# Kernel optimization log

Measured on AMD Instinct MI355X. Metric: run time of the kernel, lower is better.

## Reference

```python
import jax, jax.numpy as jnp
import numpy as np

WIN_SIZE = 256
PATCH_SIZE = [8]
CHANNEL = 32
B_CH = 256        # B_outer(8) * CHANNEL(32)
H, E = 8, 64


def _attn(q, k):
    # q, k: [B*ch, L, H, E] -> softmax scores [B*ch, H, L, L]
    scale = 1.0 / jnp.sqrt(jnp.asarray(E, q.dtype))
    scores = jnp.einsum('blhe,bshe->bhls', q, k) * scale
    return jax.nn.softmax(scores, axis=-1)  # dropout is identity in eval


def _channel_mean(a):
    # '(b reduce_b) l m n -> b l m n' mean with reduce_b=CHANNEL (channel innermost)
    bc, h, m, n = a.shape
    return a.reshape(bc // CHANNEL, CHANNEL, h, m, n).mean(axis=1)


def setup_inputs() -> dict:
    key = jax.random.key(0)
    k1, k2, k3, k4 = jax.random.split(key, 4)
    p = PATCH_SIZE[0]
    patch_num = WIN_SIZE // p
    return {
        'queries_patch_size': jax.random.normal(k1, (B_CH, patch_num, H, E), jnp.float32),
        'keys_patch_size':    jax.random.normal(k2, (B_CH, patch_num, H, E), jnp.float32),
        'queries_patch_num':  jax.random.normal(k3, (B_CH, p, H, E), jnp.float32),
        'keys_patch_num':     jax.random.normal(k4, (B_CH, p, H, E), jnp.float32),
        'patch_index': 0,
        'attn_mask': 0,
    }


def reference(queries_patch_size, keys_patch_size, queries_patch_num, keys_patch_num, patch_index, attn_mask):
    p = PATCH_SIZE[patch_index]
    rep = WIN_SIZE // p

    # patch_size branch: element-wise repeat (einops repeat) then channel mean.
    # mean over channel commutes with the repeat, so reduce first (same math,
    # avoids the 536MB intermediate the torch code materializes).
    s_ps = _channel_mean(_attn(queries_patch_size, keys_patch_size))  # [B,H,rep,rep]
    s_ps = jnp.repeat(jnp.repeat(s_ps, p, axis=2), p, axis=3)

    # patch_num branch: torch .repeat == tile, then channel mean (also commutes).
    s_pn = _channel_mean(_attn(queries_patch_num, keys_patch_num))    # [B,H,p,p]
    s_pn = jnp.tile(s_pn, (1, 1, rep, rep))

    return (s_ps, s_pn)
```

## Files before the change

kernel.cpp:

```cpp
#include <hip/hip_runtime.h>
#include <stdint.h>


__global__ __launch_bounds__(256)
void scores_kernel(const float* __restrict__ qps,
                   const float* __restrict__ kps,
                   const float* __restrict__ qpn,
                   const float* __restrict__ kpn,
                   float* __restrict__ ws_ps,
                   float* __restrict__ ws_pn)
{
    __shared__ float red[4][32 * 36];
    const int tid  = threadIdx.x;
    const int wv   = tid >> 6;
    const int lane = tid & 63;
    const int blk  = blockIdx.x;

    if (blk < 512) {
        const int a     = blk >> 3;
        const int chunk = blk & 7;
        const int bo = a >> 3, h = a & 7;
        const int ch = chunk * 4 + wv;
        const int b  = bo * 32 + ch;
        const int i = lane >> 3, j = lane & 7;

        const float4* Q = reinterpret_cast<const float4*>(qps) + ((b * 32 + 4 * i) * 8 + h) * 16;
        const float4* K = reinterpret_cast<const float4*>(kps) + ((b * 32 + 4 * j) * 8 + h) * 16;

        float acc[4][4];
        #pragma unroll
        for (int r = 0; r < 4; ++r)
            #pragma unroll
            for (int c = 0; c < 4; ++c) acc[r][c] = 0.f;

        #pragma unroll 4
        for (int c = 0; c < 16; ++c) {
            float4 q[4], k[4];
            #pragma unroll
            for (int r = 0; r < 4; ++r) { q[r] = Q[r * 128 + c]; k[r] = K[r * 128 + c]; }
            #pragma unroll
            for (int r = 0; r < 4; ++r)
                #pragma unroll
                for (int u = 0; u < 4; ++u) {
                    acc[r][u] = fmaf(q[r].x, k[u].x, acc[r][u]);
                    acc[r][u] = fmaf(q[r].y, k[u].y, acc[r][u]);
                    acc[r][u] = fmaf(q[r].z, k[u].z, acc[r][u]);
                    acc[r][u] = fmaf(q[r].w, k[u].w, acc[r][u]);
                }
        }

        #pragma unroll
        for (int r = 0; r < 4; ++r) {
            float v0 = acc[r][0] * 0.125f, v1 = acc[r][1] * 0.125f;
            float v2 = acc[r][2] * 0.125f, v3 = acc[r][3] * 0.125f;
            float m = fmaxf(fmaxf(v0, v1), fmaxf(v2, v3));
            m = fmaxf(m, __shfl_xor(m, 1));
            m = fmaxf(m, __shfl_xor(m, 2));
            m = fmaxf(m, __shfl_xor(m, 4));
            float e0 = __expf(v0 - m), e1 = __expf(v1 - m);
            float e2 = __expf(v2 - m), e3 = __expf(v3 - m);
            float s = (e0 + e1) + (e2 + e3);
            s += __shfl_xor(s, 1);
            s += __shfl_xor(s, 2);
            s += __shfl_xor(s, 4);
            const float inv = 1.f / (s * 32.f);
            float4 p; p.x = e0 * inv; p.y = e1 * inv; p.z = e2 * inv; p.w = e3 * inv;
            *reinterpret_cast<float4*>(&red[wv][(4 * i + r) * 36 + 4 * j]) = p;
        }
        __syncthreads();

        const int l = tid >> 3, s4 = (tid & 7) * 4;
        const float4 u0 = *reinterpret_cast<const float4*>(&red[0][l * 36 + s4]);
        const float4 u1 = *reinterpret_cast<const float4*>(&red[1][l * 36 + s4]);
        const float4 u2 = *reinterpret_cast<const float4*>(&red[2][l * 36 + s4]);
        const float4 u3 = *reinterpret_cast<const float4*>(&red[3][l * 36 + s4]);
        float* dst = ws_ps + a * 1024 + tid * 4;
        unsafeAtomicAdd(dst + 0, (u0.x + u1.x) + (u2.x + u3.x));
        unsafeAtomicAdd(dst + 1, (u0.y + u1.y) + (u2.y + u3.y));
        unsafeAtomicAdd(dst + 2, (u0.z + u1.z) + (u2.z + u3.z));
        unsafeAtomicAdd(dst + 3, (u0.w + u1.w) + (u2.w + u3.w));
    } else {
        const int pid = (blk - 512) * 4 + wv;
        const int b = pid >> 3, h = pid & 7;
        const int i = lane >> 3, j = lane & 7;
        const float4* qv = reinterpret_cast<const float4*>(qpn) + ((b * 8 + i) * 8 + h) * 16;
        const float4* kv = reinterpret_cast<const float4*>(kpn) + ((b * 8 + j) * 8 + h) * 16;

        float acc = 0.f;
        #pragma unroll
        for (int c = 0; c < 16; ++c) {
            float4 q = qv[c], k = kv[c];
            acc = fmaf(q.x, k.x, acc);
            acc = fmaf(q.y, k.y, acc);
            acc = fmaf(q.z, k.z, acc);
            acc = fmaf(q.w, k.w, acc);
        }
        const float s = acc * 0.125f;
        float m = s;
        m = fmaxf(m, __shfl_xor(m, 1));
        m = fmaxf(m, __shfl_xor(m, 2));
        m = fmaxf(m, __shfl_xor(m, 4));
        float e = __expf(s - m);
        float sum = e;
        sum += __shfl_xor(sum, 1);
        sum += __shfl_xor(sum, 2);
        sum += __shfl_xor(sum, 4);
        unsafeAtomicAdd(ws_pn + ((b >> 5) * 8 + h) * 64 + lane, e / (sum * 32.f));
    }
}

__global__ __launch_bounds__(256)
void writer_kernel(const float* __restrict__ ws_ps,
                   const float* __restrict__ ws_pn,
                   float* __restrict__ out)
{
    const int g = blockIdx.x * 256 + threadIdx.x;
    float4* o4 = reinterpret_cast<float4*>(out);
    if (g < 1048576) {
        const int a  = g >> 14;
        const int r  = g & 16383;
        const int i  = r >> 6;
        const int j4 = r & 63;
        const float v = ws_ps[a * 1024 + (i >> 3) * 32 + (j4 >> 1)];
        float4 o; o.x = v; o.y = v; o.z = v; o.w = v;
        o4[g] = o;
    } else {
        const int g2 = g - 1048576;
        const int a  = g2 >> 14;
        const int r  = g2 & 16383;
        const int i  = r >> 6;
        const int j4 = r & 63;
        o4[g] = *reinterpret_cast<const float4*>(ws_pn + a * 64 + (i & 7) * 8 + 4 * (j4 & 1));
    }
}

extern "C" void kernel_launch(void* const* d_in, const int* in_sizes, int n_in,
                              void* d_out, int out_size, void* d_ws, size_t ws_size,
                              hipStream_t stream) {
    const float *qps = nullptr, *kps = nullptr, *qpn = nullptr, *kpn = nullptr;
    for (int idx = 0; idx < n_in; ++idx) {
        if (in_sizes[idx] == 256 * 32 * 8 * 64) {
            if (!qps) qps = (const float*)d_in[idx];
            else if (!kps) kps = (const float*)d_in[idx];
        } else if (in_sizes[idx] == 256 * 8 * 8 * 64) {
            if (!qpn) qpn = (const float*)d_in[idx];
            else if (!kpn) kpn = (const float*)d_in[idx];
        }
    }

    float* ws_ps = (float*)d_ws;
    float* ws_pn = ws_ps + 64 * 1024;

    hipMemsetAsync(d_ws, 0, (64 * 1024 + 64 * 64) * sizeof(float), stream);
    scores_kernel<<<1024, 256, 0, stream>>>(qps, kps, qpn, kpn, ws_ps, ws_pn);
    writer_kernel<<<8192, 256, 0, stream>>>(ws_ps, ws_pn, (float*)d_out);
}
```

Measured before the change: 122.1 us.

## Replace atomic channel reduction with per-chunk partials summed in writer

Each scores block now writes its partial channel sum to a dedicated workspace slot with a plain vector store instead of global atomics, and the patch_num branch first reduces its four waves in shared memory. The writer kernel sums the eight chunk partials when it expands the output, so the workspace memset is no longer needed. This removes atomic contention and one memset launch, but the writer does eight times more reads per output element. Those reads are mostly cache hits.

Result: no change. 120.8 us (-1.0%).

```diff
diff --git a/kernel.cpp b/kernel.cpp
--- a/kernel.cpp
+++ b/kernel.cpp
@@ -74,14 +74,18 @@
         const float4 u1 = *reinterpret_cast<const float4*>(&red[1][l * 36 + s4]);
         const float4 u2 = *reinterpret_cast<const float4*>(&red[2][l * 36 + s4]);
         const float4 u3 = *reinterpret_cast<const float4*>(&red[3][l * 36 + s4]);
-        float* dst = ws_ps + a * 1024 + tid * 4;
-        unsafeAtomicAdd(dst + 0, (u0.x + u1.x) + (u2.x + u3.x));
-        unsafeAtomicAdd(dst + 1, (u0.y + u1.y) + (u2.y + u3.y));
-        unsafeAtomicAdd(dst + 2, (u0.z + u1.z) + (u2.z + u3.z));
-        unsafeAtomicAdd(dst + 3, (u0.w + u1.w) + (u2.w + u3.w));
+        float4 o;
+        o.x = (u0.x + u1.x) + (u2.x + u3.x);
+        o.y = (u0.y + u1.y) + (u2.y + u3.y);
+        o.z = (u0.z + u1.z) + (u2.z + u3.z);
+        o.w = (u0.w + u1.w) + (u2.w + u3.w);
+        reinterpret_cast<float4*>(ws_ps + (a * 8 + chunk) * 1024)[tid] = o;
     } else {
-        const int pid = (blk - 512) * 4 + wv;
-        const int b = pid >> 3, h = pid & 7;
+        const int bb    = blk - 512;
+        const int a2    = bb >> 3;
+        const int chunk = bb & 7;
+        const int bo = a2 >> 3, h = a2 & 7;
+        const int b  = bo * 32 + chunk * 4 + wv;
         const int i = lane >> 3, j = lane & 7;
         const float4* qv = reinterpret_cast<const float4*>(qpn) + ((b * 8 + i) * 8 + h) * 16;
         const float4* kv = reinterpret_cast<const float4*>(kpn) + ((b * 8 + j) * 8 + h) * 16;
@@ -105,7 +109,13 @@
         sum += __shfl_xor(sum, 1);
         sum += __shfl_xor(sum, 2);
         sum += __shfl_xor(sum, 4);
-        unsafeAtomicAdd(ws_pn + ((b >> 5) * 8 + h) * 64 + lane, e / (sum * 32.f));
+
+        red[wv][lane] = e / (sum * 32.f);
+        __syncthreads();
+        if (tid < 64) {
+            ws_pn[(a2 * 8 + chunk) * 64 + tid] =
+                (red[0][tid] + red[1][tid]) + (red[2][tid] + red[3][tid]);
+        }
     }
 }
 
@@ -121,7 +131,10 @@
         const int r  = g & 16383;
         const int i  = r >> 6;
         const int j4 = r & 63;
-        const float v = ws_ps[a * 1024 + (i >> 3) * 32 + (j4 >> 1)];
+        const float* base = ws_ps + a * 8192 + (i >> 3) * 32 + (j4 >> 1);
+        float v = 0.f;
+        #pragma unroll
+        for (int k = 0; k < 8; ++k) v += base[k * 1024];
         float4 o; o.x = v; o.y = v; o.z = v; o.w = v;
         o4[g] = o;
     } else {
@@ -130,7 +143,14 @@
         const int r  = g2 & 16383;
         const int i  = r >> 6;
         const int j4 = r & 63;
-        o4[g] = *reinterpret_cast<const float4*>(ws_pn + a * 64 + (i & 7) * 8 + 4 * (j4 & 1));
+        const float* base = ws_pn + a * 512 + (i & 7) * 8 + 4 * (j4 & 1);
+        float4 v = {0.f, 0.f, 0.f, 0.f};
+        #pragma unroll
+        for (int k = 0; k < 8; ++k) {
+            const float4 p = *reinterpret_cast<const float4*>(base + k * 64);
+            v.x += p.x; v.y += p.y; v.z += p.z; v.w += p.w;
+        }
+        o4[g] = v;
     }
 }
 
@@ -149,9 +169,8 @@
     }
 
     float* ws_ps = (float*)d_ws;
-    float* ws_pn = ws_ps + 64 * 1024;
+    float* ws_pn = ws_ps + 64 * 8 * 1024;
 
-    hipMemsetAsync(d_ws, 0, (64 * 1024 + 64 * 64) * sizeof(float), stream);
     scores_kernel<<<1024, 256, 0, stream>>>(qps, kps, qpn, kpn, ws_ps, ws_pn);
     writer_kernel<<<8192, 256, 0, stream>>>(ws_ps, ws_pn, (float*)d_out);
 }
```
